# Kernel optimization log

Measured on AMD Instinct MI355X. Metric: run time of the kernel, lower is better.

Reference implementation:

```python
import jax, jax.numpy as jnp
import numpy as np

# YOLOv1 config constants
GRIDS = 7
CLASSES = 20
IMAGE_SIZE = 448.0
LAMBDA_COOR = 5.0
LAMBDA_NOOBJ = 0.5
FEAT = 5 + CLASSES  # 25


def _make_target(bboxes):
    """bboxes: (B, n, 5) pixel coords [x1,y1,x2,y2,label] -> target (B,G,G,25).
    First-write-wins per grid cell, matching the torch per-box loop."""
    B, n, _ = bboxes.shape
    box = bboxes[..., :4] / IMAGE_SIZE                      # (B,n,4) in [0,1]
    label = bboxes[..., 4].astype(jnp.int32)                # (B,n)
    xc = (box[..., 0] + box[..., 2]) * 0.5
    yc = (box[..., 1] + box[..., 3]) * 0.5
    w = box[..., 2] - box[..., 0]
    h = box[..., 3] - box[..., 1]
    xg = jnp.floor(xc * GRIDS).astype(jnp.int32)
    yg = jnp.floor(yc * GRIDS).astype(jnp.int32)
    xo = xc * GRIDS - xg
    yo = yc * GRIDS - yg
    cell = yg * GRIDS + xg                                  # (B,n) flat cell id
    # first-come-first-serve: drop box j if an earlier box k<j hit the same cell
    same = cell[:, :, None] == cell[:, None, :]             # (B,n,n)
    earlier = jnp.tril(jnp.ones((n, n), dtype=bool), k=-1)
    keep = ~jnp.any(same & earlier, axis=-1)                # (B,n)
    one_hot = jax.nn.one_hot(label, CLASSES, dtype=jnp.float32)
    vals = jnp.concatenate(
        [xo[..., None], yo[..., None], w[..., None], h[..., None],
         jnp.ones_like(xo)[..., None], one_hot], axis=-1)   # (B,n,25)
    # route dropped boxes to an out-of-range index -> scatter drops them;
    # kept boxes have unique cells per image so .set is deterministic
    flat_idx = jnp.arange(B, dtype=jnp.int32)[:, None] * (GRIDS * GRIDS) + cell
    flat_idx = jnp.where(keep, flat_idx, B * GRIDS * GRIDS)  # OOB sentinel
    target = jnp.zeros((B * GRIDS * GRIDS, FEAT), dtype=jnp.float32)
    target = target.at[flat_idx.reshape(-1)].set(
        vals.reshape(-1, FEAT), mode='drop')
    return target.reshape(B, GRIDS, GRIDS, FEAT)


def reference(pred, bboxes):
    target = _make_target(bboxes)
    obj_mask = target[:, :, :, 4]
    noobj_mask = (1.0 - obj_mask) * LAMBDA_NOOBJ
    loss_contain = (target[:, :, :, 4] - pred[:, :, :, 4]) ** 2
    loss_contain = ((obj_mask + noobj_mask) * loss_contain).sum((1, 2))
    loss_coord = ((target[:, :, :, 0] - pred[:, :, :, 0]) ** 2
                  + (target[:, :, :, 1] - pred[:, :, :, 1]) ** 2
                  + (jnp.sqrt(target[:, :, :, 2]) - jnp.sqrt(pred[:, :, :, 2])) ** 2
                  + (jnp.sqrt(target[:, :, :, 3]) - jnp.sqrt(pred[:, :, :, 3])) ** 2)
    loss_coord = (obj_mask * loss_coord * LAMBDA_COOR).sum((1, 2))
    loss_class = (target[:, :, :, 5:] - pred[:, :, :, 5:]) ** 2
    loss_class = (obj_mask[..., None] * loss_class).sum((1, 2, 3))
    return (loss_contain + loss_coord + loss_class).mean()


def setup_inputs() -> dict:
    key = jax.random.key(0)
    k1, k2, k3, k4, k5 = jax.random.split(key, 5)
    B, n = 16384, 8
    # pred in (0.05, 0.95) so sqrt of w/h channels is well-defined
    pred = jax.random.uniform(k1, (B, GRIDS, GRIDS, FEAT), dtype=jnp.float32) * 0.9 + 0.05
    # valid boxes in pixels: centers in (0.25,0.75)*448, sizes in (0.05,0.4)*448
    cx = (jax.random.uniform(k2, (B, n)) * 0.5 + 0.25) * IMAGE_SIZE
    cy = (jax.random.uniform(k3, (B, n)) * 0.5 + 0.25) * IMAGE_SIZE
    wh = (jax.random.uniform(k4, (B, n, 2)) * 0.35 + 0.05) * IMAGE_SIZE
    x1 = cx - wh[..., 0] * 0.5
    x2 = cx + wh[..., 0] * 0.5
    y1 = cy - wh[..., 1] * 0.5
    y2 = cy + wh[..., 1] * 0.5
    label = jax.random.randint(k5, (B, n), 0, CLASSES).astype(jnp.float32)
    bboxes = jnp.stack([x1, y1, x2, y2, label], axis=-1).astype(jnp.float32)
    return {"pred": pred, "bboxes": bboxes}
```

## Files before the change

### kernel.cpp

```cpp
#include <hip/hip_runtime.h>

#define GRIDS 7
#define NCELL 49
#define NFEAT 25
#define CELLSZ 1225
#define BPB 8
#define MAXBOX 16


__global__ __launch_bounds__(256) void yolo_main(
    const float* __restrict__ pred, const float* __restrict__ bbox,
    float* __restrict__ partial, int B, int nbox)
{
    __shared__ float sBox[BPB * MAXBOX * 5];
    __shared__ int   sCell[BPB * MAXBOX];
    __shared__ int   sKeep[BPB * MAXBOX];
    __shared__ float sRed[4];

    const int tid = threadIdx.x;
    const long long b0 = (long long)blockIdx.x * BPB;
    const int nb = min(BPB, B - (int)b0);
    const int nbx = nb * nbox;

    if (tid < nbx) {
        const float* bx = bbox + (b0 * nbox + tid) * 5;
        float x1 = bx[0] / 448.f, y1 = bx[1] / 448.f;
        float x2 = bx[2] / 448.f, y2 = bx[3] / 448.f;
        float xc = (x1 + x2) * 0.5f, yc = (y1 + y2) * 0.5f;
        float w  = x2 - x1,          h  = y2 - y1;
        float xs = xc * (float)GRIDS, ys = yc * (float)GRIDS;
        float xg = floorf(xs), yg = floorf(ys);
        sCell[tid] = (int)yg * GRIDS + (int)xg;
        float* e = &sBox[tid * 5];
        e[0] = xs - xg; e[1] = ys - yg;
        e[2] = sqrtf(w); e[3] = sqrtf(h);
        e[4] = bx[4];
    }
    __syncthreads();

    if (tid < nbx) {
        int lb = tid / nbox;
        int c  = sCell[tid];
        int k = 1;
        for (int i = lb * nbox; i < tid; ++i)
            if (sCell[i] == c) { k = 0; break; }
        sKeep[tid] = k;
    }
    __syncthreads();

    const int nelem = nb * CELLSZ;
    const int nvec  = nelem >> 2;
    const float* pb = pred + b0 * CELLSZ;
    const float4* p4 = (const float4*)pb;
    float acc = 0.f;
    int i = tid;
    for (; i + 256 < nvec; i += 512) {
        float4 a = p4[i];
        float4 b = p4[i + 256];
        {
            unsigned e0 = (unsigned)i << 2;
            unsigned q = (e0 * 5243u) >> 17;
            unsigned r = e0 - q * 25u;
            float c = (r == 4u) ? a.x : (r == 3u) ? a.y : (r == 2u) ? a.z
                    : (r == 1u) ? a.w : 0.f;
            acc = fmaf(0.5f * c, c, acc);
        }
        {
            unsigned e0 = (unsigned)(i + 256) << 2;
            unsigned q = (e0 * 5243u) >> 17;
            unsigned r = e0 - q * 25u;
            float c = (r == 4u) ? b.x : (r == 3u) ? b.y : (r == 2u) ? b.z
                    : (r == 1u) ? b.w : 0.f;
            acc = fmaf(0.5f * c, c, acc);
        }
    }
    if (i < nvec) {
        float4 a = p4[i];
        unsigned e0 = (unsigned)i << 2;
        unsigned q = (e0 * 5243u) >> 17;
        unsigned r = e0 - q * 25u;
        float c = (r == 4u) ? a.x : (r == 3u) ? a.y : (r == 2u) ? a.z
                : (r == 1u) ? a.w : 0.f;
        acc = fmaf(0.5f * c, c, acc);
    }
    for (int e = (nvec << 2) + tid; e < nelem; e += 256) {
        unsigned q = ((unsigned)e * 5243u) >> 17;
        if ((unsigned)e - q * 25u == 4u) {
            float p = pb[e];
            acc = fmaf(0.5f * p, p, acc);
        }
    }

    for (int t = tid; t < nbx * NFEAT; t += 256) {
        unsigned bi = ((unsigned)t * 5243u) >> 17;
        int f = t - (int)bi * NFEAT;
        if (sKeep[bi]) {
            int lb = (int)bi / nbox;
            const float* e = &sBox[bi * 5];
            float p = pb[lb * CELLSZ + sCell[bi] * NFEAT + f];
            float term;
            if (f < 2) {
                float d = e[f] - p;           term = 5.f * d * d;
            } else if (f < 4) {
                float d = e[f] - sqrtf(p);    term = 5.f * d * d;
            } else if (f == 4) {
                float d = 1.f - p;            term = d * d - 0.5f * p * p;
            } else {
                float tt = ((int)e[4] == f - 5) ? 1.f : 0.f;
                float d = tt - p;             term = d * d;
            }
            acc += term;
        }
    }

    for (int off = 32; off; off >>= 1)
        acc += __shfl_down(acc, off, 64);
    if ((tid & 63) == 0) sRed[tid >> 6] = acc;
    __syncthreads();
    if (tid == 0)
        partial[blockIdx.x] = sRed[0] + sRed[1] + sRed[2] + sRed[3];
}

__global__ __launch_bounds__(256) void yolo_reduce(
    const float* __restrict__ partial, int n, float* __restrict__ out, int B)
{
    __shared__ double s[256];
    double a = 0.0;
    for (int i = threadIdx.x; i < n; i += 256) a += (double)partial[i];
    s[threadIdx.x] = a;
    __syncthreads();
    for (int str = 128; str; str >>= 1) {
        if (threadIdx.x < str) s[threadIdx.x] += s[threadIdx.x + str];
        __syncthreads();
    }
    if (threadIdx.x == 0) out[0] = (float)(s[0] / (double)B);
}

extern "C" void kernel_launch(void* const* d_in, const int* in_sizes, int n_in,
                              void* d_out, int out_size, void* d_ws, size_t ws_size,
                              hipStream_t stream) {
    const float* pred = (const float*)d_in[0];
    const float* bbox = (const float*)d_in[1];
    int B = in_sizes[0] / CELLSZ;
    int nbox = in_sizes[1] / (B * 5);
    if (nbox > MAXBOX) nbox = MAXBOX;
    float* out = (float*)d_out;
    float* partial = (float*)d_ws;

    int nblocks = (B + BPB - 1) / BPB;
    yolo_main<<<nblocks, 256, 0, stream>>>(pred, bbox, partial, B, nbox);
    yolo_reduce<<<1, 256, 0, stream>>>(partial, nblocks, out, B);
}
```

Measured before the change: 26.79 us.

## Fuse final reduction into main kernel via last-block atomic counter

Merges the separate single-block reduce kernel into the main kernel: each block writes its partial sum, increments a global counter, and the last block reduces all partials in double precision. It also remaps the per-box gather so each half-wave handles one box's 25 features, and precomputes the flat pred offset per box. This removes one kernel launch but adds a memset launch, a threadfence and atomic per block, and a serialized tail reduction in one block.

```diff
diff --git a/kernel.cpp b/kernel.cpp
--- a/kernel.cpp
+++ b/kernel.cpp
@@ -8,14 +8,17 @@
 #define MAXBOX 16
 
 
-__global__ __launch_bounds__(256) void yolo_main(
+__global__ __launch_bounds__(256) void yolo_fused(
     const float* __restrict__ pred, const float* __restrict__ bbox,
-    float* __restrict__ partial, int B, int nbox)
+    float* __restrict__ partial, unsigned* __restrict__ counter,
+    float* __restrict__ out, int B, int nbox, int nblocks)
 {
-    __shared__ float sBox[BPB * MAXBOX * 5];
-    __shared__ int   sCell[BPB * MAXBOX];
-    __shared__ int   sKeep[BPB * MAXBOX];
-    __shared__ float sRed[4];
+    __shared__ float  sBox[BPB * MAXBOX * 5];
+    __shared__ int    sOff[BPB * MAXBOX];
+    __shared__ int    sKeep[BPB * MAXBOX];
+    __shared__ float  sRed[4];
+    __shared__ double sRedD[256];
+    __shared__ int    sLast;
 
     const int tid = threadIdx.x;
     const long long b0 = (long long)blockIdx.x * BPB;
@@ -30,7 +33,9 @@
         float w  = x2 - x1,          h  = y2 - y1;
         float xs = xc * (float)GRIDS, ys = yc * (float)GRIDS;
         float xg = floorf(xs), yg = floorf(ys);
-        sCell[tid] = (int)yg * GRIDS + (int)xg;
+        int lb = tid / nbox;
+        int cell = (int)yg * GRIDS + (int)xg;
+        sOff[tid] = lb * CELLSZ + cell * NFEAT;
         float* e = &sBox[tid * 5];
         e[0] = xs - xg; e[1] = ys - yg;
         e[2] = sqrtf(w); e[3] = sqrtf(h);
@@ -40,10 +45,10 @@
 
     if (tid < nbx) {
         int lb = tid / nbox;
-        int c  = sCell[tid];
+        int o  = sOff[tid];
         int k = 1;
         for (int i = lb * nbox; i < tid; ++i)
-            if (sCell[i] == c) { k = 0; break; }
+            if (sOff[i] == o) { k = 0; break; }
         sKeep[tid] = k;
     }
     __syncthreads();
@@ -91,25 +96,28 @@
         }
     }
 
-    for (int t = tid; t < nbx * NFEAT; t += 256) {
-        unsigned bi = ((unsigned)t * 5243u) >> 17;
-        int f = t - (int)bi * NFEAT;
-        if (sKeep[bi]) {
-            int lb = (int)bi / nbox;
-            const float* e = &sBox[bi * 5];
-            float p = pb[lb * CELLSZ + sCell[bi] * NFEAT + f];
-            float term;
-            if (f < 2) {
-                float d = e[f] - p;           term = 5.f * d * d;
-            } else if (f < 4) {
-                float d = e[f] - sqrtf(p);    term = 5.f * d * d;
-            } else if (f == 4) {
-                float d = 1.f - p;            term = d * d - 0.5f * p * p;
-            } else {
-                float tt = ((int)e[4] == f - 5) ? 1.f : 0.f;
-                float d = tt - p;             term = d * d;
+    {
+        const int wid = tid >> 6, lane = tid & 63;
+        const int f = lane & 31;
+        for (int bi = wid * 2 + (lane >> 5); bi < nbx; bi += 8) {
+            if (f < NFEAT && sKeep[bi]) {
+                const float* e = &sBox[bi * 5];
+                float p = pb[sOff[bi] + f];
+                float term;
+                if (f == 4) {
+                    float d = 1.f - p;
+                    term = fmaf(d, d, -0.5f * p * p);
+                } else if (f < 4) {
+                    float q = (f >= 2) ? sqrtf(p) : p;
+                    float d = e[f] - q;
+                    term = 5.f * d * d;
+                } else {
+                    float t = ((int)e[4] == f - 5) ? 1.f : 0.f;
+                    float d = t - p;
+                    term = d * d;
+                }
+                acc += term;
             }
-            acc += term;
         }
     }
 
@@ -117,23 +125,28 @@
         acc += __shfl_down(acc, off, 64);
     if ((tid & 63) == 0) sRed[tid >> 6] = acc;
     __syncthreads();
-    if (tid == 0)
+
+    if (tid == 0) {
         partial[blockIdx.x] = sRed[0] + sRed[1] + sRed[2] + sRed[3];
-}
-
-__global__ __launch_bounds__(256) void yolo_reduce(
-    const float* __restrict__ partial, int n, float* __restrict__ out, int B)
-{
-    __shared__ double s[256];
-    double a = 0.0;
-    for (int i = threadIdx.x; i < n; i += 256) a += (double)partial[i];
-    s[threadIdx.x] = a;
+        __threadfence();
+        unsigned prev = __hip_atomic_fetch_add(counter, 1u, __ATOMIC_ACQ_REL,
+                                               __HIP_MEMORY_SCOPE_AGENT);
+        sLast = (prev == (unsigned)(nblocks - 1));
+    }
     __syncthreads();
-    for (int str = 128; str; str >>= 1) {
-        if (threadIdx.x < str) s[threadIdx.x] += s[threadIdx.x + str];
+    if (sLast) {
+        double a = 0.0;
+        for (int j = tid; j < nblocks; j += 256)
+            a += (double)__hip_atomic_load(&partial[j], __ATOMIC_RELAXED,
+                                           __HIP_MEMORY_SCOPE_AGENT);
+        sRedD[tid] = a;
         __syncthreads();
+        for (int s = 128; s; s >>= 1) {
+            if (tid < s) sRedD[tid] += sRedD[tid + s];
+            __syncthreads();
+        }
+        if (tid == 0) out[0] = (float)(sRedD[0] / (double)B);
     }
-    if (threadIdx.x == 0) out[0] = (float)(s[0] / (double)B);
 }
 
 extern "C" void kernel_launch(void* const* d_in, const int* in_sizes, int n_in,
@@ -145,9 +158,12 @@
     int nbox = in_sizes[1] / (B * 5);
     if (nbox > MAXBOX) nbox = MAXBOX;
     float* out = (float*)d_out;
-    float* partial = (float*)d_ws;
 
     int nblocks = (B + BPB - 1) / BPB;
-    yolo_main<<<nblocks, 256, 0, stream>>>(pred, bbox, partial, B, nbox);
-    yolo_reduce<<<1, 256, 0, stream>>>(partial, nblocks, out, B);
+    float* partial = (float*)d_ws;
+    unsigned* counter = (unsigned*)((char*)d_ws + (size_t)nblocks * sizeof(float));
+
+    hipMemsetAsync(counter, 0, sizeof(unsigned), stream);
+    yolo_fused<<<nblocks, 256, 0, stream>>>(pred, bbox, partial, counter, out,
+                                            B, nbox, nblocks);
 }
```

Measured after the change: 91.23 us. +240.6%, slower.
